# Kernel optimization log

Measured on AMD Instinct MI355X. Metric: run time of the kernel, lower is better.

The kernel has to match this reference:

```python
import jax, jax.numpy as jnp
import numpy as np

N_HEADS = 32
N_KV = 8
HEAD_DIM = 64
GROUP = N_HEADS // N_KV  # 4


def setup_inputs() -> dict:
    key = jax.random.key(0)
    ks = jax.random.split(key, 6)
    b, s, d_in, d_out = 1, 4096, 2048, 2048
    d_kv = N_KV * HEAD_DIM
    sc = 0.02
    return {
        'x': jax.random.normal(ks[0], (b, s, d_in), jnp.float32),
        'Wq': jax.random.normal(ks[1], (d_in, d_out), jnp.float32) * sc,
        'Wk': jax.random.normal(ks[2], (d_in, d_kv), jnp.float32) * sc,
        'Wv': jax.random.normal(ks[3], (d_in, d_kv), jnp.float32) * sc,
        'Wo': jax.random.normal(ks[4], (d_out, d_out), jnp.float32) * sc,
        'bo': jnp.zeros((d_out,), jnp.float32),
    }


def reference(x, Wq, Wk, Wv, Wo, bo):
    b, s, _ = x.shape
    # projections (no qkv bias)
    q = (x @ Wq).reshape(b, s, N_HEADS, HEAD_DIM).transpose(0, 2, 1, 3)  # [b,h,s,hd]
    k = (x @ Wk).reshape(b, s, N_KV, HEAD_DIM).transpose(0, 2, 1, 3)    # [b,g,s,hd]
    v = (x @ Wv).reshape(b, s, N_KV, HEAD_DIM).transpose(0, 2, 1, 3)
    # GQA: repeat kv heads (matches repeat_interleave on dim=1)
    k = jnp.repeat(k, GROUP, axis=1)  # [b,h,s,hd]
    v = jnp.repeat(v, GROUP, axis=1)
    scores = jnp.einsum('bhqd,bhkd->bhqk', q, k)
    causal = jnp.triu(jnp.ones((s, s), dtype=bool), k=1)
    scores = jnp.where(causal, -jnp.inf, scores)
    attn = jax.nn.softmax(scores / (HEAD_DIM ** 0.5), axis=-1)
    ctx = jnp.einsum('bhqk,bhkd->bhqd', attn, v)
    ctx = ctx.transpose(0, 2, 1, 3).reshape(b, s, N_HEADS * HEAD_DIM)
    return ctx @ Wo + bo
```

## Files before the change

kernel.cpp:

```cpp
#include <hip/hip_runtime.h>
#include <hip/hip_bf16.h>
#include <cstdint>


typedef unsigned int u32;
typedef unsigned short u16;
typedef __attribute__((ext_vector_type(8))) short bf16x8;
typedef __attribute__((ext_vector_type(4))) float f32x4;
typedef __attribute__((ext_vector_type(2))) u32 u32x2;

typedef __attribute__((address_space(3))) void lds_void_t;
typedef __attribute__((address_space(1))) void gbl_void_t;

__device__ __forceinline__ void gload_lds16(const u16* g, u16* l) {
    __builtin_amdgcn_global_load_lds((const gbl_void_t*)g, (lds_void_t*)l, 16, 0, 0);
}

__device__ __forceinline__ u16 f2bf(float f) {
    union { float f; u32 i; } c; c.f = f;
    return (u16)((c.i + 0x7fffu + ((c.i >> 16) & 1u)) >> 16);
}
__device__ __forceinline__ float bfround(float f) {
    union { float f; u32 i; } c; c.f = f;
    c.i = (c.i + 0x7fffu + ((c.i >> 16) & 1u)) & 0xffff0000u;
    return c.f;
}
__device__ __forceinline__ u32 packbf2(float a, float b) {
    union { __hip_bfloat162 h; u32 w; } c;
    c.h = __float22bfloat162_rn(make_float2(a, b));
    return c.w;
}

__global__ __launch_bounds__(256) void cast_f2b_kernel(
    const float* __restrict__ s, u16* __restrict__ d)
{
    int i = (blockIdx.x * 256 + threadIdx.x) * 8;
    float4 a = *reinterpret_cast<const float4*>(s + i);
    float4 b = *reinterpret_cast<const float4*>(s + i + 4);
    u32 w[4];
    w[0] = packbf2(a.x, a.y); w[1] = packbf2(a.z, a.w);
    w[2] = packbf2(b.x, b.y); w[3] = packbf2(b.z, b.w);
    *reinterpret_cast<uint4*>(d + i) = *reinterpret_cast<const uint4*>(w);
}

__global__ __launch_bounds__(256) void cast_transpose_kernel(
    const float* __restrict__ W, u16* __restrict__ Wt, int K, int N)
{
    __shared__ float tile[64][65];
    const int k0 = blockIdx.y * 64, n0 = blockIdx.x * 64;
    const int t = threadIdx.x;
#pragma unroll
    for (int i = 0; i < 16; ++i) {
        int idx = t + i * 256;
        int r = idx >> 6, c = idx & 63;
        tile[r][c] = W[(size_t)(k0 + r) * N + n0 + c];
    }
    __syncthreads();
#pragma unroll
    for (int i = 0; i < 16; ++i) {
        int idx = t + i * 256;
        int r = idx >> 6, c = idx & 63;
        Wt[(size_t)(n0 + r) * K + k0 + c] = f2bf(tile[c][r]);
    }
}

__global__ __launch_bounds__(256) void gemm_qkv_kernel(
    const u16* __restrict__ A, const u16* __restrict__ Bt,
    u16* __restrict__ Qw, u16* __restrict__ Kw, u16* __restrict__ Vtw,
    int M, int K, float qscale)
{
    __shared__ __align__(16) u16 As[128][32];
    __shared__ __align__(16) u16 Bs[128][32];

    const int tid  = threadIdx.x;
    const int wave = tid >> 6;
    const int lane = tid & 63;
    const int col  = lane & 15;
    const int quad = lane >> 4;
    const int bm = blockIdx.y * 128, bn = blockIdx.x * 128;
    const int mhalf = (wave & 1) * 64, nhalf = (wave >> 1) * 64;

    const int srow = wave * 32 + (lane >> 2);
    const int skch = lane & 3;
    const u16* ga = A  + (size_t)(bm + srow) * K + skch * 8;
    const u16* gb = Bt + (size_t)(bn + srow) * K + skch * 8;
    u16* lA0 = &As[wave * 32][0];
    u16* lA1 = &As[wave * 32 + 16][0];
    u16* lB0 = &Bs[wave * 32][0];
    u16* lB1 = &Bs[wave * 32 + 16][0];

    f32x4 acc[4][4];
#pragma unroll
    for (int i = 0; i < 4; ++i)
#pragma unroll
        for (int j = 0; j < 4; ++j) acc[i][j] = (f32x4){0.f, 0.f, 0.f, 0.f};

    for (int k0 = 0; k0 < K; k0 += 32) {
        __syncthreads();
        gload_lds16(ga, lA0);
        gload_lds16(ga + 16 * K, lA1);
        gload_lds16(gb, lB0);
        gload_lds16(gb + 16 * K, lB1);
        ga += 32; gb += 32;
        __syncthreads();

        bf16x8 af[4], bf[4];
#pragma unroll
        for (int t = 0; t < 4; ++t)
            af[t] = *reinterpret_cast<const bf16x8*>(&As[mhalf + t * 16 + col][quad * 8]);
#pragma unroll
        for (int t = 0; t < 4; ++t)
            bf[t] = *reinterpret_cast<const bf16x8*>(&Bs[nhalf + t * 16 + col][quad * 8]);
#pragma unroll
        for (int tm = 0; tm < 4; ++tm)
#pragma unroll
            for (int tn = 0; tn < 4; ++tn)
                acc[tm][tn] = __builtin_amdgcn_mfma_f32_16x16x32_bf16(
                    af[tm], bf[tn], acc[tm][tn], 0, 0, 0);
    }

    if (bn < 2048) {
#pragma unroll
        for (int tm = 0; tm < 4; ++tm) {
            int row0 = bm + mhalf + tm * 16 + quad * 4;
#pragma unroll
            for (int r = 0; r < 4; ++r) {
                u16* cp = Qw + (size_t)(row0 + r) * 2048 + bn + nhalf + col;
#pragma unroll
                for (int tn = 0; tn < 4; ++tn)
                    cp[tn * 16] = f2bf(acc[tm][tn][r] * qscale);
            }
        }
    } else if (bn < 2560) {
        const int cb = bn - 2048;
#pragma unroll
        for (int tm = 0; tm < 4; ++tm) {
            int row0 = bm + mhalf + tm * 16 + quad * 4;
#pragma unroll
            for (int r = 0; r < 4; ++r) {
                u16* cp = Kw + (size_t)(row0 + r) * 512 + cb + nhalf + col;
#pragma unroll
                for (int tn = 0; tn < 4; ++tn)
                    cp[tn * 16] = f2bf(acc[tm][tn][r]);
            }
        }
    } else {
        const int cb = bn - 2560;
#pragma unroll
        for (int tn = 0; tn < 4; ++tn) {
            int nrow = cb + nhalf + tn * 16 + col;
#pragma unroll
            for (int tm = 0; tm < 4; ++tm) {
                int m0 = bm + mhalf + tm * 16 + quad * 4;
                ushort4 v;
                v.x = f2bf(acc[tm][tn][0]); v.y = f2bf(acc[tm][tn][1]);
                v.z = f2bf(acc[tm][tn][2]); v.w = f2bf(acc[tm][tn][3]);
                *reinterpret_cast<ushort4*>(&Vtw[(size_t)nrow * M + m0]) = v;
            }
        }
    }
}

__global__ __launch_bounds__(256) void gemm_out_kernel(
    const u16* __restrict__ A, const u16* __restrict__ Bt,
    const float* __restrict__ bias, float* __restrict__ Co,
    int M, int N, int K)
{
    __shared__ __align__(16) u16 As[128][32];
    __shared__ __align__(16) u16 Bs[128][32];

    const int tid  = threadIdx.x;
    const int wave = tid >> 6;
    const int lane = tid & 63;
    const int col  = lane & 15;
    const int quad = lane >> 4;
    const int bm = blockIdx.y * 128, bn = blockIdx.x * 128;
    const int mhalf = (wave & 1) * 64, nhalf = (wave >> 1) * 64;

    const int srow = wave * 32 + (lane >> 2);
    const int skch = lane & 3;
    const u16* ga = A  + (size_t)(bm + srow) * K + skch * 8;
    const u16* gb = Bt + (size_t)(bn + srow) * K + skch * 8;
    u16* lA0 = &As[wave * 32][0];
    u16* lA1 = &As[wave * 32 + 16][0];
    u16* lB0 = &Bs[wave * 32][0];
    u16* lB1 = &Bs[wave * 32 + 16][0];

    f32x4 acc[4][4];
#pragma unroll
    for (int i = 0; i < 4; ++i)
#pragma unroll
        for (int j = 0; j < 4; ++j) acc[i][j] = (f32x4){0.f, 0.f, 0.f, 0.f};

    for (int k0 = 0; k0 < K; k0 += 32) {
        __syncthreads();
        gload_lds16(ga, lA0);
        gload_lds16(ga + 16 * K, lA1);
        gload_lds16(gb, lB0);
        gload_lds16(gb + 16 * K, lB1);
        ga += 32; gb += 32;
        __syncthreads();

        bf16x8 af[4], bf[4];
#pragma unroll
        for (int t = 0; t < 4; ++t)
            af[t] = *reinterpret_cast<const bf16x8*>(&As[mhalf + t * 16 + col][quad * 8]);
#pragma unroll
        for (int t = 0; t < 4; ++t)
            bf[t] = *reinterpret_cast<const bf16x8*>(&Bs[nhalf + t * 16 + col][quad * 8]);
#pragma unroll
        for (int tm = 0; tm < 4; ++tm)
#pragma unroll
            for (int tn = 0; tn < 4; ++tn)
                acc[tm][tn] = __builtin_amdgcn_mfma_f32_16x16x32_bf16(
                    af[tm], bf[tn], acc[tm][tn], 0, 0, 0);
    }

    float bj[4];
#pragma unroll
    for (int tn = 0; tn < 4; ++tn) bj[tn] = bias[bn + nhalf + tn * 16 + col];
#pragma unroll
    for (int tm = 0; tm < 4; ++tm) {
        int row0 = bm + mhalf + tm * 16 + quad * 4;
#pragma unroll
        for (int r = 0; r < 4; ++r) {
            float* cp = Co + (size_t)(row0 + r) * N + bn + nhalf + col;
#pragma unroll
            for (int tn = 0; tn < 4; ++tn)
                cp[tn * 16] = bfround(acc[tm][tn][r] + bj[tn]);
        }
    }
}

__global__ __launch_bounds__(256, 2) void attn_mfma_kernel(
    const u16* __restrict__ Q,
    const u16* __restrict__ Kd,
    const u16* __restrict__ Vt,
    u16* __restrict__ CTX,
    int S)
{
    __shared__ __align__(16) u16 Ks[2][64][64];
    __shared__ __align__(16) u16 Vs[2][64][64];
    __shared__ __align__(16) u32 Pu[4][1024];

    const int pairi = blockIdx.x;
    const int h    = blockIdx.y;
    const int g    = h >> 2;
    const int tid  = threadIdx.x;
    const int wave = tid >> 6;
    const int lane = tid & 63;
    const int col  = lane & 15;
    const int quad = lane >> 4;

    const int srow8 = lane >> 3;
    const int schk  = (lane & 7) ^ srow8;
    const u16* gK = Kd + (size_t)(wave * 16 + srow8) * 512 + g * 64 + schk * 8;
    const u16* gV = Vt + (size_t)(g * 64 + wave * 16 + srow8) * 4096 + schk * 8;

    const int wbase = ((quad >> 1) * 16 + col) * 4 + (quad & 1) * 2;

#pragma unroll 1
    for (int pass = 0; pass < 2; ++pass) {
        const int qt = pass ? pairi : (31 - pairi);
        const int qb = qt * 128;

        bf16x8 qf[2][2];
#pragma unroll
        for (int mt = 0; mt < 2; ++mt) {
            const u16* qp = Q + (size_t)(qb + wave * 32 + mt * 16 + col) * 2048
                            + h * 64 + quad * 8;
            qf[mt][0] = *reinterpret_cast<const bf16x8*>(qp);
            qf[mt][1] = *reinterpret_cast<const bf16x8*>(qp + 32);
        }

        f32x4 o_acc[2][4];
        float l_acc[2];
#pragma unroll
        for (int mt = 0; mt < 2; ++mt) {
            l_acc[mt] = 0.f;
#pragma unroll
            for (int t = 0; t < 4; ++t)
                o_acc[mt][t] = (f32x4){0.f, 0.f, 0.f, 0.f};
        }

        const int ktmax = 2 * qt + 1;

        gload_lds16(gK, &Ks[0][wave * 16][0]);
        gload_lds16(gK + (size_t)8 * 512, &Ks[0][wave * 16 + 8][0]);
        gload_lds16(gV, &Vs[0][wave * 16][0]);
        gload_lds16(gV + 8 * 4096, &Vs[0][wave * 16 + 8][0]);

        for (int kt = 0; kt <= ktmax; ++kt) {
            const int kbase = kt * 64;
            const int cur = kt & 1;
            __syncthreads();

            if (kt < ktmax) {
                const int nb = cur ^ 1;
                const size_t ko = (size_t)(kbase + 64);
                gload_lds16(gK + ko * 512, &Ks[nb][wave * 16][0]);
                gload_lds16(gK + (ko + 8) * 512, &Ks[nb][wave * 16 + 8][0]);
                gload_lds16(gV + ko, &Vs[nb][wave * 16][0]);
                gload_lds16(gV + 8 * 4096 + ko, &Vs[nb][wave * 16 + 8][0]);
            }

            const int base0 = qb + wave * 32;
            if (kbase > base0 + 31) continue;
            const bool act0 = (kbase <= base0 + 15);

            f32x4 sc0[4], sc1[4];
#pragma unroll
            for (int t = 0; t < 4; ++t) {
                const int krow = t * 16 + col;
                bf16x8 k0 = *reinterpret_cast<const bf16x8*>(
                    &Ks[cur][krow][((quad    ) ^ (krow & 7)) * 8]);
                bf16x8 k1 = *reinterpret_cast<const bf16x8*>(
                    &Ks[cur][krow][((quad + 4) ^ (krow & 7)) * 8]);
                f32x4 c4 = {-16.f, -16.f, -16.f, -16.f};
                c4 = __builtin_amdgcn_mfma_f32_16x16x32_bf16(k0, qf[1][0], c4, 0, 0, 0);
                c4 = __builtin_amdgcn_mfma_f32_16x16x32_bf16(k1, qf[1][1], c4, 0, 0, 0);
                sc1[t] = c4;
                if (act0) {
                    f32x4 d4 = {-16.f, -16.f, -16.f, -16.f};
                    d4 = __builtin_amdgcn_mfma_f32_16x16x32_bf16(k0, qf[0][0], d4, 0, 0, 0);
                    d4 = __builtin_amdgcn_mfma_f32_16x16x32_bf16(k1, qf[0][1], d4, 0, 0, 0);
                    sc0[t] = d4;
                }
            }

            if (kbase + 63 > base0) {
#pragma unroll
                for (int t = 0; t < 4; ++t) {
                    const int keyq = kbase + t * 16 + quad * 4;
#pragma unroll
                    for (int r = 0; r < 4; ++r) {
                        if (keyq + r > base0 + 16 + col) sc1[t][r] = -1e30f;
                        if (act0 && (keyq + r > base0 + col)) sc0[t][r] = -1e30f;
                    }
                }
            }

            {
                float ls0 = 0.f, ls1 = 0.f;
#pragma unroll
                for (int t = 0; t < 4; ++t) {
                    float p0 = __builtin_amdgcn_exp2f(sc1[t][0]);
                    float p1 = __builtin_amdgcn_exp2f(sc1[t][1]);
                    float p2 = __builtin_amdgcn_exp2f(sc1[t][2]);
                    float p3 = __builtin_amdgcn_exp2f(sc1[t][3]);
                    ls1 += (p0 + p1) + (p2 + p3);
                    u32x2 w;
                    w.x = packbf2(p0, p1);
                    w.y = packbf2(p2, p3);
                    *reinterpret_cast<u32x2*>(&Pu[wave][512 + wbase + t * 128]) = w;
                    if (act0) {
                        float q0 = __builtin_amdgcn_exp2f(sc0[t][0]);
                        float q1 = __builtin_amdgcn_exp2f(sc0[t][1]);
                        float q2 = __builtin_amdgcn_exp2f(sc0[t][2]);
                        float q3 = __builtin_amdgcn_exp2f(sc0[t][3]);
                        ls0 += (q0 + q1) + (q2 + q3);
                        u32x2 v;
                        v.x = packbf2(q0, q1);
                        v.y = packbf2(q2, q3);
                        *reinterpret_cast<u32x2*>(&Pu[wave][wbase + t * 128]) = v;
                    }
                }
                l_acc[1] += ls1;
                if (act0) l_acc[0] += ls0;
            }

            __builtin_amdgcn_s_waitcnt(0xC07F);
            __builtin_amdgcn_wave_barrier();

            bf16x8 pa1_0 = *reinterpret_cast<const bf16x8*>(&Pu[wave][512 + lane * 4]);
            bf16x8 pa1_1 = *reinterpret_cast<const bf16x8*>(&Pu[wave][768 + lane * 4]);
            bf16x8 pa0_0, pa0_1;
            if (act0) {
                pa0_0 = *reinterpret_cast<const bf16x8*>(&Pu[wave][lane * 4]);
                pa0_1 = *reinterpret_cast<const bf16x8*>(&Pu[wave][256 + lane * 4]);
            }

#pragma unroll
            for (int t = 0; t < 4; ++t) {
                const int d = t * 16 + col;
                bf16x8 vb0 = *reinterpret_cast<const bf16x8*>(
                    &Vs[cur][d][((quad    ) ^ (d & 7)) * 8]);
                bf16x8 vb1 = *reinterpret_cast<const bf16x8*>(
                    &Vs[cur][d][((quad + 4) ^ (d & 7)) * 8]);
                o_acc[1][t] = __builtin_amdgcn_mfma_f32_16x16x32_bf16(pa1_0, vb0, o_acc[1][t], 0, 0, 0);
                o_acc[1][t] = __builtin_amdgcn_mfma_f32_16x16x32_bf16(pa1_1, vb1, o_acc[1][t], 0, 0, 0);
                if (act0) {
                    o_acc[0][t] = __builtin_amdgcn_mfma_f32_16x16x32_bf16(pa0_0, vb0, o_acc[0][t], 0, 0, 0);
                    o_acc[0][t] = __builtin_amdgcn_mfma_f32_16x16x32_bf16(pa0_1, vb1, o_acc[0][t], 0, 0, 0);
                }
            }
        }

#pragma unroll
        for (int mt = 0; mt < 2; ++mt) {
            float v = l_acc[mt];
            v += __shfl_xor(v, 16, 64);
            v += __shfl_xor(v, 32, 64);
            const int src0 = (lane & 48) + ((lane >> 4) & 3) * 4;
#pragma unroll
            for (int r = 0; r < 4; ++r) {
                const float lv = __shfl(v, src0 + r, 64);
                const float inv = 1.f / lv;
                const int row = qb + wave * 32 + mt * 16 + quad * 4 + r;
                u16* cp = CTX + (size_t)row * 2048 + h * 64;
#pragma unroll
                for (int t = 0; t < 4; ++t)
                    cp[t * 16 + col] = f2bf(o_acc[mt][t][r] * inv);
            }
        }
    }
}

extern "C" void kernel_launch(void* const* d_in, const int* in_sizes, int n_in,
                              void* d_out, int out_size, void* d_ws, size_t ws_size,
                              hipStream_t stream)
{
    const float* x  = (const float*)d_in[0];
    const float* Wq = (const float*)d_in[1];
    const float* Wk = (const float*)d_in[2];
    const float* Wv = (const float*)d_in[3];
    const float* Wo = (const float*)d_in[4];
    const float* bo = (const float*)d_in[5];
    float* out = (float*)d_out;

    const int S = 4096, Din = 2048, Dq = 2048, Dkv = 512;
    const float QSCALE = 0.125f * 1.44269504f;

    u16* xb  = (u16*)d_ws;
    u16* Qw  = xb + (size_t)S * Din;
    u16* Kw  = Qw + (size_t)S * Dq;
    u16* Vtw = Kw + (size_t)S * Dkv;
    u16* Cw   = xb;
    u16* Wobt = Qw;

    u16* Wqkvt = (u16*)d_out;

    dim3 blk(256);
    cast_f2b_kernel<<<dim3((S * Din) / (256 * 8)), blk, 0, stream>>>(x, xb);
    cast_transpose_kernel<<<dim3(Dq  / 64, Din / 64), blk, 0, stream>>>(Wq, Wqkvt, Din, Dq);
    cast_transpose_kernel<<<dim3(Dkv / 64, Din / 64), blk, 0, stream>>>(Wk, Wqkvt + (size_t)2048 * Din, Din, Dkv);
    cast_transpose_kernel<<<dim3(Dkv / 64, Din / 64), blk, 0, stream>>>(Wv, Wqkvt + (size_t)2560 * Din, Din, Dkv);

    gemm_qkv_kernel<<<dim3(3072 / 128, S / 128), blk, 0, stream>>>(
        xb, Wqkvt, Qw, Kw, Vtw, S, Din, QSCALE);

    attn_mfma_kernel<<<dim3(16, 32), blk, 0, stream>>>(Qw, Kw, Vtw, Cw, S);

    cast_transpose_kernel<<<dim3(Dq / 64, Dq / 64), blk, 0, stream>>>(Wo, Wobt, Dq, Dq);
    gemm_out_kernel<<<dim3(Dq / 128, S / 128), blk, 0, stream>>>(Cw, Wobt, bo, out, S, Dq, Dq);
}
```

Before: 364.5 us.

## Double-buffer LDS tiles in QKV and output GEMMs to overlap loads with MFMA

Both GEMM kernels now use two LDS buffers per operand. The first K-tile is prefetched before the loop, and each iteration issues the global-to-LDS loads for the next tile before computing on the current one. This drops one of the two barriers per iteration and hides global load latency behind the MFMA work. In exchange, LDS use per block doubles, which may lower occupancy. Correctness relies on the barrier waiting for the outstanding async LDS loads.

```diff
diff --git a/kernel.cpp b/kernel.cpp
--- a/kernel.cpp
+++ b/kernel.cpp
@@ -69,8 +69,8 @@
     u16* __restrict__ Qw, u16* __restrict__ Kw, u16* __restrict__ Vtw,
     int M, int K, float qscale)
 {
-    __shared__ __align__(16) u16 As[128][32];
-    __shared__ __align__(16) u16 Bs[128][32];
+    __shared__ __align__(16) u16 As[2][128][32];
+    __shared__ __align__(16) u16 Bs[2][128][32];
 
     const int tid  = threadIdx.x;
     const int wave = tid >> 6;
@@ -84,10 +84,7 @@
     const int skch = lane & 3;
     const u16* ga = A  + (size_t)(bm + srow) * K + skch * 8;
     const u16* gb = Bt + (size_t)(bn + srow) * K + skch * 8;
-    u16* lA0 = &As[wave * 32][0];
-    u16* lA1 = &As[wave * 32 + 16][0];
-    u16* lB0 = &Bs[wave * 32][0];
-    u16* lB1 = &Bs[wave * 32 + 16][0];
+    const int w32 = wave * 32;
 
     f32x4 acc[4][4];
 #pragma unroll
@@ -95,22 +92,32 @@
 #pragma unroll
         for (int j = 0; j < 4; ++j) acc[i][j] = (f32x4){0.f, 0.f, 0.f, 0.f};
 
+    gload_lds16(ga, &As[0][w32][0]);
+    gload_lds16(ga + 16 * K, &As[0][w32 + 16][0]);
+    gload_lds16(gb, &Bs[0][w32][0]);
+    gload_lds16(gb + 16 * K, &Bs[0][w32 + 16][0]);
+    ga += 32; gb += 32;
+
     for (int k0 = 0; k0 < K; k0 += 32) {
+        const int cur = (k0 >> 5) & 1;
         __syncthreads();
-        gload_lds16(ga, lA0);
-        gload_lds16(ga + 16 * K, lA1);
-        gload_lds16(gb, lB0);
-        gload_lds16(gb + 16 * K, lB1);
-        ga += 32; gb += 32;
-        __syncthreads();
+
+        if (k0 + 32 < K) {
+            const int nb = cur ^ 1;
+            gload_lds16(ga, &As[nb][w32][0]);
+            gload_lds16(ga + 16 * K, &As[nb][w32 + 16][0]);
+            gload_lds16(gb, &Bs[nb][w32][0]);
+            gload_lds16(gb + 16 * K, &Bs[nb][w32 + 16][0]);
+            ga += 32; gb += 32;
+        }
 
         bf16x8 af[4], bf[4];
 #pragma unroll
         for (int t = 0; t < 4; ++t)
-            af[t] = *reinterpret_cast<const bf16x8*>(&As[mhalf + t * 16 + col][quad * 8]);
+            af[t] = *reinterpret_cast<const bf16x8*>(&As[cur][mhalf + t * 16 + col][quad * 8]);
 #pragma unroll
         for (int t = 0; t < 4; ++t)
-            bf[t] = *reinterpret_cast<const bf16x8*>(&Bs[nhalf + t * 16 + col][quad * 8]);
+            bf[t] = *reinterpret_cast<const bf16x8*>(&Bs[cur][nhalf + t * 16 + col][quad * 8]);
 #pragma unroll
         for (int tm = 0; tm < 4; ++tm)
 #pragma unroll
@@ -166,8 +173,8 @@
     const float* __restrict__ bias, float* __restrict__ Co,
     int M, int N, int K)
 {
-    __shared__ __align__(16) u16 As[128][32];
-    __shared__ __align__(16) u16 Bs[128][32];
+    __shared__ __align__(16) u16 As[2][128][32];
+    __shared__ __align__(16) u16 Bs[2][128][32];
 
     const int tid  = threadIdx.x;
     const int wave = tid >> 6;
@@ -181,10 +188,7 @@
     const int skch = lane & 3;
     const u16* ga = A  + (size_t)(bm + srow) * K + skch * 8;
     const u16* gb = Bt + (size_t)(bn + srow) * K + skch * 8;
-    u16* lA0 = &As[wave * 32][0];
-    u16* lA1 = &As[wave * 32 + 16][0];
-    u16* lB0 = &Bs[wave * 32][0];
-    u16* lB1 = &Bs[wave * 32 + 16][0];
+    const int w32 = wave * 32;
 
     f32x4 acc[4][4];
 #pragma unroll
@@ -192,22 +196,32 @@
 #pragma unroll
         for (int j = 0; j < 4; ++j) acc[i][j] = (f32x4){0.f, 0.f, 0.f, 0.f};
 
+    gload_lds16(ga, &As[0][w32][0]);
+    gload_lds16(ga + 16 * K, &As[0][w32 + 16][0]);
+    gload_lds16(gb, &Bs[0][w32][0]);
+    gload_lds16(gb + 16 * K, &Bs[0][w32 + 16][0]);
+    ga += 32; gb += 32;
+
     for (int k0 = 0; k0 < K; k0 += 32) {
+        const int cur = (k0 >> 5) & 1;
         __syncthreads();
-        gload_lds16(ga, lA0);
-        gload_lds16(ga + 16 * K, lA1);
-        gload_lds16(gb, lB0);
-        gload_lds16(gb + 16 * K, lB1);
-        ga += 32; gb += 32;
-        __syncthreads();
+
+        if (k0 + 32 < K) {
+            const int nb = cur ^ 1;
+            gload_lds16(ga, &As[nb][w32][0]);
+            gload_lds16(ga + 16 * K, &As[nb][w32 + 16][0]);
+            gload_lds16(gb, &Bs[nb][w32][0]);
+            gload_lds16(gb + 16 * K, &Bs[nb][w32 + 16][0]);
+            ga += 32; gb += 32;
+        }
 
         bf16x8 af[4], bf[4];
 #pragma unroll
         for (int t = 0; t < 4; ++t)
-            af[t] = *reinterpret_cast<const bf16x8*>(&As[mhalf + t * 16 + col][quad * 8]);
+            af[t] = *reinterpret_cast<const bf16x8*>(&As[cur][mhalf + t * 16 + col][quad * 8]);
 #pragma unroll
         for (int t = 0; t < 4; ++t)
-            bf[t] = *reinterpret_cast<const bf16x8*>(&Bs[nhalf + t * 16 + col][quad * 8]);
+            bf[t] = *reinterpret_cast<const bf16x8*>(&Bs[cur][nhalf + t * 16 + col][quad * 8]);
 #pragma unroll
         for (int tm = 0; tm < 4; ++tm)
 #pragma unroll
```

Measured after the change: 341.8 us. 1.07x faster.
